# Optimization experiments

Measured on AMD Instinct MI355X. Metric: run time of the kernel, lower is better.

## Reference

```python
import jax, jax.numpy as jnp
import numpy as np

DIM_IN = 16
DIM_OUT = 64

def setup_inputs() -> dict:
    key = jax.random.key(0)
    ks = jax.random.split(key, 7)
    B, T, N = 4, 8, 256
    s_in = 1.0 / np.sqrt(DIM_IN)
    s_out = 1.0 / np.sqrt(DIM_OUT)
    return {
        "query": jax.random.normal(ks[0], (B, N, DIM_IN), dtype=jnp.float32),
        "keys": jax.random.normal(ks[1], (B, T, N, DIM_IN), dtype=jnp.float32),
        "Wq": jax.random.uniform(ks[2], (DIM_IN, DIM_OUT), jnp.float32, -s_in, s_in),
        "bq": jax.random.uniform(ks[3], (DIM_OUT,), jnp.float32, -s_in, s_in),
        "Wk": jax.random.uniform(ks[4], (DIM_IN, DIM_OUT), jnp.float32, -s_in, s_in),
        "bk": jax.random.uniform(ks[5], (DIM_OUT,), jnp.float32, -s_in, s_in),
        "wt": jax.random.uniform(ks[6], (DIM_OUT,), jnp.float32, -s_out, s_out),
    }

def reference(query, keys, Wq, bq, Wk, bk, wt):
    # q: [B, N, D] -> [B, 1, N, 1, D]
    q = (jnp.einsum('bnf,fd->bnd', query, Wq) + bq)[:, None, :, None, :]
    # k: [B, T, N, D] -> [B, T, 1, N, D]
    k = (jnp.einsum('btnf,fd->btnd', keys, Wk) + bk)[:, :, None, :, :]
    # scores: [B, T, N, N] via tanh of broadcast add, reduced by wt
    scores = jnp.einsum('btnmd,d->btnm', jnp.tanh(q + k), wt)
    return jax.nn.softmax(scores, axis=-1)
```

## Files before the change

kernel.cpp:

```cpp
#include <hip/hip_runtime.h>

#define B_ 4
#define T_ 8
#define N_ 256
#define F_ 16
#define D_ 64
#define NP (D_/2)
#define CHUNK 8
#define NCH (N_/CHUNK)

#define SC 2.8853900817779268f
#define LOG2E 1.4426950408889634f

__device__ __forceinline__ float fast_exp2(float x) { return __builtin_amdgcn_exp2f(x); }
__device__ __forceinline__ float fast_rcp(float x)  { return __builtin_amdgcn_rcpf(x); }

__global__ __launch_bounds__(256)
void tattn_proj_kernel(const float* __restrict__ query,
                       const float* __restrict__ keys,
                       const float* __restrict__ Wq, const float* __restrict__ bq,
                       const float* __restrict__ Wk, const float* __restrict__ bk,
                       float* __restrict__ Eq, float* __restrict__ Ek)
{
    const int tid = threadIdx.x;
    const int row = blockIdx.x * 4 + (tid >> 6);
    const int j   = tid & 63;
    const int NQ  = B_ * N_;

    const float* in; const float* W; const float* bias; float* outp;
    if (row < NQ) {
        in   = query + (size_t)row * F_;
        W    = Wq;  bias = bq;
        outp = Eq + (size_t)row * D_;
    } else {
        int r = row - NQ;
        in   = keys + (size_t)r * F_;
        W    = Wk;  bias = bk;
        outp = Ek + (size_t)r * D_;
    }
    float acc = bias[j];
    #pragma unroll
    for (int f = 0; f < F_; ++f)
        acc = fmaf(in[f], W[f * D_ + j], acc);
    outp[j] = fast_exp2(acc * SC);
}

__global__ __launch_bounds__(256, 4)
void tattn_main_kernel(const float* __restrict__ Eq,
                       const float* __restrict__ Ek,
                       const float* __restrict__ wt,
                       float* __restrict__ out)
{
    __shared__ float4 comb[CHUNK][NP];
    __shared__ float  pbuf[CHUNK][N_];
    __shared__ float  partial[CHUNK][4];

    const int tid = threadIdx.x;
    const int bid = blockIdx.x;
    const int ch  = bid % NCH;
    const int t   = (bid / NCH) % T_;
    const int b   = bid / (NCH * T_);
    const int n0  = ch * CHUNK;

    float kreg[D_];
    {
        const float* kp = Ek + (((size_t)(b * T_ + t)) * N_ + tid) * D_;
        #pragma unroll
        for (int d = 0; d < D_; d += 4) {
            float4 v = *reinterpret_cast<const float4*>(kp + d);
            kreg[d] = v.x; kreg[d+1] = v.y; kreg[d+2] = v.z; kreg[d+3] = v.w;
        }
    }

    {
        const int nn = tid >> 5, pr = tid & 31;
        float2 e2 = *reinterpret_cast<const float2*>(Eq + ((size_t)b * N_ + n0 + nn) * D_ + 2 * pr);
        float2 w2 = *reinterpret_cast<const float2*>(wt + 2 * pr);
        comb[nn][pr] = make_float4(e2.x, e2.y, 2.0f * w2.x, 2.0f * w2.y);
    }

    float Wsum = 0.f;
    #pragma unroll
    for (int d = 0; d < D_; ++d) Wsum += wt[d];

    __syncthreads();

    const int lane = tid & 63;
    const int wid  = tid >> 6;

    #pragma unroll 1
    for (int nn = 0; nn < CHUNK; ++nn) {
        float acc[4] = {0.f, 0.f, 0.f, 0.f};
        #pragma unroll
        for (int pr = 0; pr < NP; ++pr) {
            float4 c = comb[nn][pr];
            float pA = fmaf(c.x, kreg[2*pr+0], 1.0f);
            float qA = fmaf(c.y, kreg[2*pr+1], 1.0f);
            float nA = c.z * qA;
            nA = fmaf(c.w, pA, nA);
            acc[pr & 3] = fmaf(nA, fast_rcp(pA * qA), acc[pr & 3]);
        }
        float score = Wsum - ((acc[0] + acc[1]) + (acc[2] + acc[3]));

        float pv = fast_exp2(score * LOG2E);
        pbuf[nn][tid] = pv;
        float s = pv;
        #pragma unroll
        for (int off = 32; off >= 1; off >>= 1) s += __shfl_xor(s, off);
        if (lane == 0) partial[nn][wid] = s;
    }
    __syncthreads();

    const size_t obase = ((size_t)((b * T_ + t) * N_ + n0)) * N_ + tid;
    #pragma unroll
    for (int nn = 0; nn < CHUNK; ++nn) {
        float tot = (partial[nn][0] + partial[nn][1]) + (partial[nn][2] + partial[nn][3]);
        out[obase + (size_t)nn * N_] = pbuf[nn][tid] * fast_rcp(tot);
    }
}

extern "C" void kernel_launch(void* const* d_in, const int* in_sizes, int n_in,
                              void* d_out, int out_size, void* d_ws, size_t ws_size,
                              hipStream_t stream) {
    const float* query = (const float*)d_in[0];
    const float* keys  = (const float*)d_in[1];
    const float* Wq    = (const float*)d_in[2];
    const float* bq    = (const float*)d_in[3];
    const float* Wk    = (const float*)d_in[4];
    const float* bk    = (const float*)d_in[5];
    const float* wt    = (const float*)d_in[6];
    float* out = (float*)d_out;

    float* Eq = (float*)d_ws;
    float* Ek = Eq + (size_t)B_ * N_ * D_;

    const int rows = B_ * N_ + B_ * T_ * N_;
    hipLaunchKernelGGL(tattn_proj_kernel, dim3(rows / 4), dim3(256), 0, stream,
                       query, keys, Wq, bq, Wk, bk, Eq, Ek);

    hipLaunchKernelGGL(tattn_main_kernel, dim3(B_ * T_ * NCH), dim3(256), 0, stream,
                       Eq, Ek, wt, out);
}
```

Before: 32.10 us.

## Precompute packed query/weight float4s in projection kernel and drop shared staging

The projection kernel now writes the query side straight into the packed (eq, eq_partner, 2*wt, 2*wt) float4 layout. The main kernel reads those float4s directly from global memory, where all lanes load the same uniform address, instead of staging them in LDS behind a barrier. Softmax numerators are kept in registers rather than an LDS buffer, and the chunk loop is fully unrolled. This removes one barrier and the LDS traffic, at the cost of more registers and per-iteration global/scalar loads that may have higher latency than LDS reads.

After: 41.68 us. 29.8% more time.

```diff
diff --git a/kernel.cpp b/kernel.cpp
--- a/kernel.cpp
+++ b/kernel.cpp
@@ -20,40 +20,42 @@
                        const float* __restrict__ keys,
                        const float* __restrict__ Wq, const float* __restrict__ bq,
                        const float* __restrict__ Wk, const float* __restrict__ bk,
-                       float* __restrict__ Eq, float* __restrict__ Ek)
+                       const float* __restrict__ wt,
+                       float4* __restrict__ combG, float* __restrict__ Ek)
 {
     const int tid = threadIdx.x;
     const int row = blockIdx.x * 4 + (tid >> 6);
     const int j   = tid & 63;
     const int NQ  = B_ * N_;
 
-    const float* in; const float* W; const float* bias; float* outp;
     if (row < NQ) {
-        in   = query + (size_t)row * F_;
-        W    = Wq;  bias = bq;
-        outp = Eq + (size_t)row * D_;
+        const float* in = query + (size_t)row * F_;
+        float acc = bq[j];
+        #pragma unroll
+        for (int f = 0; f < F_; ++f) acc = fmaf(in[f], Wq[f * D_ + j], acc);
+        float eq = fast_exp2(acc * SC);
+        float partner = __shfl_xor(eq, 1);
+        if ((j & 1) == 0) {
+            combG[(size_t)row * NP + (j >> 1)] =
+                make_float4(eq, partner, 2.0f * wt[j], 2.0f * wt[j + 1]);
+        }
     } else {
-        int r = row - NQ;
-        in   = keys + (size_t)r * F_;
-        W    = Wk;  bias = bk;
-        outp = Ek + (size_t)r * D_;
+        const int r = row - NQ;
+        const float* in = keys + (size_t)r * F_;
+        float acc = bk[j];
+        #pragma unroll
+        for (int f = 0; f < F_; ++f) acc = fmaf(in[f], Wk[f * D_ + j], acc);
+        Ek[(size_t)r * D_ + j] = fast_exp2(acc * SC);
     }
-    float acc = bias[j];
-    #pragma unroll
-    for (int f = 0; f < F_; ++f)
-        acc = fmaf(in[f], W[f * D_ + j], acc);
-    outp[j] = fast_exp2(acc * SC);
 }
 
 __global__ __launch_bounds__(256, 4)
-void tattn_main_kernel(const float* __restrict__ Eq,
+void tattn_main_kernel(const float4* __restrict__ combG,
                        const float* __restrict__ Ek,
                        const float* __restrict__ wt,
                        float* __restrict__ out)
 {
-    __shared__ float4 comb[CHUNK][NP];
-    __shared__ float  pbuf[CHUNK][N_];
-    __shared__ float  partial[CHUNK][4];
+    __shared__ float partial[CHUNK][4];
 
     const int tid = threadIdx.x;
     const int bid = blockIdx.x;
@@ -72,39 +74,35 @@
         }
     }
 
-    {
-        const int nn = tid >> 5, pr = tid & 31;
-        float2 e2 = *reinterpret_cast<const float2*>(Eq + ((size_t)b * N_ + n0 + nn) * D_ + 2 * pr);
-        float2 w2 = *reinterpret_cast<const float2*>(wt + 2 * pr);
-        comb[nn][pr] = make_float4(e2.x, e2.y, 2.0f * w2.x, 2.0f * w2.y);
-    }
-
     float Wsum = 0.f;
     #pragma unroll
     for (int d = 0; d < D_; ++d) Wsum += wt[d];
 
-    __syncthreads();
-
     const int lane = tid & 63;
     const int wid  = tid >> 6;
+    float pv[CHUNK];
 
-    #pragma unroll 1
+    #pragma unroll
     for (int nn = 0; nn < CHUNK; ++nn) {
-        float acc[4] = {0.f, 0.f, 0.f, 0.f};
+        const float4* cg = combG + ((size_t)(b * N_ + n0 + nn)) * NP;
+        float a0 = 0.f, a1 = 0.f, a2 = 0.f, a3 = 0.f;
         #pragma unroll
         for (int pr = 0; pr < NP; ++pr) {
-            float4 c = comb[nn][pr];
+            float4 c = cg[pr];
             float pA = fmaf(c.x, kreg[2*pr+0], 1.0f);
             float qA = fmaf(c.y, kreg[2*pr+1], 1.0f);
-            float nA = c.z * qA;
-            nA = fmaf(c.w, pA, nA);
-            acc[pr & 3] = fmaf(nA, fast_rcp(pA * qA), acc[pr & 3]);
+            float nA = fmaf(c.w, pA, c.z * qA);
+            float r  = fast_rcp(pA * qA);
+            if      ((pr & 3) == 0) a0 = fmaf(nA, r, a0);
+            else if ((pr & 3) == 1) a1 = fmaf(nA, r, a1);
+            else if ((pr & 3) == 2) a2 = fmaf(nA, r, a2);
+            else                    a3 = fmaf(nA, r, a3);
         }
-        float score = Wsum - ((acc[0] + acc[1]) + (acc[2] + acc[3]));
+        float score = Wsum - ((a0 + a1) + (a2 + a3));
 
-        float pv = fast_exp2(score * LOG2E);
-        pbuf[nn][tid] = pv;
-        float s = pv;
+        float p = fast_exp2(score * LOG2E);
+        pv[nn] = p;
+        float s = p;
         #pragma unroll
         for (int off = 32; off >= 1; off >>= 1) s += __shfl_xor(s, off);
         if (lane == 0) partial[nn][wid] = s;
@@ -115,7 +113,7 @@
     #pragma unroll
     for (int nn = 0; nn < CHUNK; ++nn) {
         float tot = (partial[nn][0] + partial[nn][1]) + (partial[nn][2] + partial[nn][3]);
-        out[obase + (size_t)nn * N_] = pbuf[nn][tid] * fast_rcp(tot);
+        out[obase + (size_t)nn * N_] = pv[nn] * fast_rcp(tot);
     }
 }
 
@@ -131,13 +129,13 @@
     const float* wt    = (const float*)d_in[6];
     float* out = (float*)d_out;
 
-    float* Eq = (float*)d_ws;
-    float* Ek = Eq + (size_t)B_ * N_ * D_;
+    float4* combG = (float4*)d_ws;
+    float*  Ek    = (float*)((char*)d_ws + (size_t)B_ * N_ * NP * sizeof(float4));
 
     const int rows = B_ * N_ + B_ * T_ * N_;
     hipLaunchKernelGGL(tattn_proj_kernel, dim3(rows / 4), dim3(256), 0, stream,
-                       query, keys, Wq, bq, Wk, bk, Eq, Ek);
+                       query, keys, Wq, bq, Wk, bk, wt, combG, Ek);
 
     hipLaunchKernelGGL(tattn_main_kernel, dim3(B_ * T_ * NCH), dim3(256), 0, stream,
-                       Eq, Ek, wt, out);
+                       combG, Ek, wt, out);
 }
```
